# Kernel optimization log

Hardware: AMD Instinct MI355X
Metric: run time of the kernel (lower is better)

Reference implementation:

```python
import jax, jax.numpy as jnp
import numpy as np

H = 12
DH = 64
R = 8
LN_EPS = 1e-12


def setup_inputs() -> dict:
    key = jax.random.key(0)
    ks = jax.random.split(key, 6)
    B, T, D = 32, 512, 768
    s = 0.02  # realistic init scale so softmax/LN stay well-conditioned
    return {
        "hidden_states": jax.random.normal(ks[0], (B, T, D), jnp.float32),
        "Wq": jax.random.normal(ks[1], (D, D), jnp.float32) * s,
        "bq": jnp.zeros((D,), jnp.float32),
        "Wk": jax.random.normal(ks[2], (D, D), jnp.float32) * s,
        "bk": jnp.zeros((D,), jnp.float32),
        "Wv": jax.random.normal(ks[3], (D, D), jnp.float32) * s,
        "bv": jnp.zeros((D,), jnp.float32),
        "Wo": jax.random.normal(ks[4], (D, D), jnp.float32) * s,
        "bo": jnp.zeros((D,), jnp.float32),
        "ln_g": jnp.ones((D,), jnp.float32),
        "ln_b": jnp.zeros((D,), jnp.float32),
    }


def _bipartite_indices(metric, r):
    # metric: (B, T, dh); cosine-sim bipartite matching between even (a) and odd (b) tokens
    m = metric / (jnp.linalg.norm(metric, axis=-1, keepdims=True) + 1e-6)
    a, b = m[:, ::2], m[:, 1::2]
    scores = jnp.einsum('bad,bcd->bac', a, b)  # (B, Ta, Tb)
    node_max = scores.max(axis=-1)
    node_idx = scores.argmax(axis=-1)
    node_max = node_max.at[:, 0].set(-jnp.inf)  # protect CLS (a[0])
    r = min(r, a.shape[1] - 1)
    sorted_idx = jnp.argsort(-node_max, axis=-1)  # descending
    src_idx = sorted_idx[:, :r]
    unm_idx = sorted_idx[:, r:]
    dst_idx = jnp.take_along_axis(node_idx, src_idx, axis=-1)
    return src_idx, unm_idx, dst_idx


def _merge(x, src_idx, unm_idx, dst_idx):
    # x: (B, T, C) -> (B, T - r, C); scatter-mean matched even tokens into odd tokens
    src, dst = x[:, ::2], x[:, 1::2]
    matched = jnp.take_along_axis(src, src_idx[:, :, None], axis=1)  # (B, r, C)

    def scat(d, di, mm):
        sums = jnp.zeros_like(d).at[di].add(mm)
        cnt = jnp.zeros((d.shape[0],), d.dtype).at[di].add(jnp.ones(di.shape, d.dtype))
        # torch scatter_reduce 'mean' with include_self=True: (self + sum) / (1 + count)
        return (d + sums) / (1.0 + cnt[:, None])

    dst = jax.vmap(scat)(dst, dst_idx, matched)
    unm = jnp.take_along_axis(src, unm_idx[:, :, None], axis=1)
    return jnp.concatenate([unm, dst], axis=1)


def reference(hidden_states, Wq, bq, Wk, bk, Wv, bv, Wo, bo, ln_g, ln_b):
    B, T, D = hidden_states.shape

    def split_heads(x):
        return x.reshape(B, T, H, DH).transpose(0, 2, 1, 3)  # (B, H, T, dh)

    residual = hidden_states
    q = split_heads(hidden_states @ Wq + bq)
    k = split_heads(hidden_states @ Wk + bk)
    v = split_heads(hidden_states @ Wv + bv)

    # ToMe: match on head-averaged keys (computed under no_grad in torch)
    metric = jax.lax.stop_gradient(k.mean(axis=1))  # (B, T, dh)
    src_idx, unm_idx, dst_idx = _bipartite_indices(metric, R)

    def merge_heads(x):
        Bx, Hx, Tx, dx = x.shape
        y = x.transpose(0, 2, 1, 3).reshape(Bx, Tx, Hx * dx)
        y = _merge(y, src_idx, unm_idx, dst_idx)
        return y.reshape(Bx, y.shape[1], Hx, dx).transpose(0, 2, 1, 3)

    q = merge_heads(q)
    k = merge_heads(k)
    v = merge_heads(v)
    residual = _merge(residual, src_idx, unm_idx, dst_idx)

    scores = jnp.einsum('bhqd,bhkd->bhqk', q, k) / jnp.sqrt(jnp.float32(DH))
    probs = jax.nn.softmax(scores, axis=-1)  # dropout is identity in eval
    ctx = jnp.einsum('bhqk,bhkd->bhqd', probs, v)
    T2 = ctx.shape[2]
    ctx = ctx.transpose(0, 2, 1, 3).reshape(B, T2, D)
    out = ctx @ Wo + bo

    x = out + residual
    mu = x.mean(axis=-1, keepdims=True)
    var = x.var(axis=-1, keepdims=True)
    return (x - mu) / jnp.sqrt(var + LN_EPS) * ln_g + ln_b
```

## Files before the change

kernel.cpp:

```cpp
#include <hip/hip_runtime.h>
#include <math.h>

#define BNUM 32
#define TT   512
#define DD   768
#define HH   12
#define DHH  64
#define RR   8
#define TSRC 256
#define UNM  248
#define TM   504
#define MROW 16128

typedef unsigned short u16;
typedef unsigned int   u32;
typedef __attribute__((ext_vector_type(8))) short bfrag;
typedef __attribute__((ext_vector_type(4))) float ffrag;
typedef __attribute__((ext_vector_type(2))) unsigned int u32x2;

__device__ __forceinline__ u16 f2bf(float f) {
  u32 u = __float_as_uint(f);
  u = (u + 0x7fffu + ((u >> 16) & 1u)) >> 16;
  return (u16)u;
}
__device__ __forceinline__ u32 pack2bf(float a, float b) {
  u32 ua = __float_as_uint(a), ub = __float_as_uint(b);
  ua += 0x7fffu + ((ua >> 16) & 1u);
  ub += 0x7fffu + ((ub >> 16) & 1u);
  return (ua >> 16) | (ub & 0xffff0000u);
}
__device__ __forceinline__ float bf2f(u16 v) {
  return __uint_as_float(((u32)v) << 16);
}

__device__ __forceinline__ void gl2lds16(const u16* g, u16* l) {
  __builtin_amdgcn_global_load_lds(
      (const __attribute__((address_space(1))) void*)(g),
      (__attribute__((address_space(3))) void*)(l), 16, 0, 0);
}

__global__ __launch_bounds__(256) void wkr_kernel(
    const float* __restrict__ Wk, const float* __restrict__ bk,
    float* __restrict__ Wkr, float* __restrict__ bkr) {
  int idx = blockIdx.x * 256 + threadIdx.x;
  int d = idx >> 6, j = idx & 63;
  float s = 0.f;
  #pragma unroll
  for (int h = 0; h < HH; ++h) s += Wk[(size_t)d * DD + h * DHH + j];
  Wkr[idx] = s * (1.f / 12.f);
  if (idx < 64) {
    float sb = 0.f;
    #pragma unroll
    for (int h = 0; h < HH; ++h) sb += bk[h * DHH + idx];
    bkr[idx] = sb * (1.f / 12.f);
  }
}

__global__ __launch_bounds__(256) void gemm_f32_kernel(
    const float* __restrict__ A, const float* __restrict__ W,
    const float* __restrict__ bias, float* __restrict__ C,
    int M, int N, int K) {
  __shared__ float As[32][68];
  __shared__ float Ws[32][68];
  const int t  = threadIdx.x;
  const int m0 = blockIdx.x * 64;
  const int tx = t & 15, ty = t >> 4;
  const int a_kk = t & 31;
  const int a_m  = t >> 5;
  const int w_n  = t & 63;
  const int w_k0 = t >> 6;

  float a_pre[8], w_pre[8];
  #pragma unroll
  for (int l = 0; l < 8; ++l)
    a_pre[l] = A[(size_t)(m0 + a_m + 8 * l) * K + a_kk];
  #pragma unroll
  for (int l = 0; l < 8; ++l)
    w_pre[l] = W[(size_t)(w_k0 * 8 + l) * N + w_n];

  float acc[4][4];
  #pragma unroll
  for (int i = 0; i < 4; ++i)
    #pragma unroll
    for (int j = 0; j < 4; ++j) acc[i][j] = 0.f;

  for (int k0 = 0; k0 < K; k0 += 32) {
    __syncthreads();
    #pragma unroll
    for (int l = 0; l < 8; ++l) As[a_kk][a_m + 8 * l] = a_pre[l];
    #pragma unroll
    for (int l = 0; l < 8; ++l) Ws[w_k0 * 8 + l][w_n] = w_pre[l];
    __syncthreads();
    if (k0 + 32 < K) {
      #pragma unroll
      for (int l = 0; l < 8; ++l)
        a_pre[l] = A[(size_t)(m0 + a_m + 8 * l) * K + k0 + 32 + a_kk];
      #pragma unroll
      for (int l = 0; l < 8; ++l)
        w_pre[l] = W[(size_t)(k0 + 32 + w_k0 * 8 + l) * N + w_n];
    }
    #pragma unroll
    for (int kk = 0; kk < 32; ++kk) {
      float4 a4 = *(const float4*)&As[kk][ty * 4];
      float4 w4 = *(const float4*)&Ws[kk][tx * 4];
      acc[0][0] += a4.x * w4.x; acc[0][1] += a4.x * w4.y;
      acc[0][2] += a4.x * w4.z; acc[0][3] += a4.x * w4.w;
      acc[1][0] += a4.y * w4.x; acc[1][1] += a4.y * w4.y;
      acc[1][2] += a4.y * w4.z; acc[1][3] += a4.y * w4.w;
      acc[2][0] += a4.z * w4.x; acc[2][1] += a4.z * w4.y;
      acc[2][2] += a4.z * w4.z; acc[2][3] += a4.z * w4.w;
      acc[3][0] += a4.w * w4.x; acc[3][1] += a4.w * w4.y;
      acc[3][2] += a4.w * w4.z; acc[3][3] += a4.w * w4.w;
    }
  }
  const float4 b4 = *(const float4*)&bias[tx * 4];
  #pragma unroll
  for (int i = 0; i < 4; ++i) {
    float4 v;
    v.x = acc[i][0] + b4.x; v.y = acc[i][1] + b4.y;
    v.z = acc[i][2] + b4.z; v.w = acc[i][3] + b4.w;
    *(float4*)&C[(size_t)(m0 + ty * 4 + i) * N + tx * 4] = v;
  }
}

__global__ __launch_bounds__(256) void wconv_kernel(
    const float* __restrict__ W0, const float* __restrict__ W1,
    const float* __restrict__ W2, const float* __restrict__ W3,
    u16* __restrict__ T0, u16* __restrict__ T1,
    u16* __restrict__ T2, u16* __restrict__ T3) {
  __shared__ float tile[64][65];
  int wi = blockIdx.z;
  const float* W = (wi == 0) ? W0 : (wi == 1) ? W1 : (wi == 2) ? W2 : W3;
  u16* T = (wi == 0) ? T0 : (wi == 1) ? T1 : (wi == 2) ? T2 : T3;
  int k0 = blockIdx.x * 64, n0 = blockIdx.y * 64;
  int t = threadIdx.x;
  int r = t >> 2, c4 = (t & 3) * 16;
  #pragma unroll
  for (int j = 0; j < 16; j += 4) {
    float4 v = *(const float4*)&W[(size_t)(k0 + r) * DD + n0 + c4 + j];
    tile[r][c4 + j] = v.x; tile[r][c4 + j + 1] = v.y;
    tile[r][c4 + j + 2] = v.z; tile[r][c4 + j + 3] = v.w;
  }
  __syncthreads();
  #pragma unroll
  for (int j = 0; j < 16; j += 2) {
    u32 p = (u32)f2bf(tile[c4 + j][r]) | ((u32)f2bf(tile[c4 + j + 1][r]) << 16);
    *(u32*)&T[(size_t)(n0 + r) * DD + k0 + c4 + j] = p;
  }
}

template <bool OUT_BF16, bool ADD_RES, bool ROW_BIAS, bool QK, bool ASHARE>
__global__ __launch_bounds__(256, 4) void mfma_gemm_kernel(
    const u16* __restrict__ A, const u16* __restrict__ BT,
    const float* __restrict__ bias, const float* __restrict__ bias2,
    const float* __restrict__ Res,
    float* __restrict__ Cf, u16* __restrict__ Cb, u16* __restrict__ Cb2,
    int M, int N, int K) {
  __shared__ u16 Als[2][128 * 32];
  __shared__ u16 Bls[2][128 * 32];
  const int t  = threadIdx.x;

  const int gx = gridDim.x, gy = gridDim.y;
  const int nwg = gx * gy;
  int id = blockIdx.x + blockIdx.y * gx;
  {
    const int qq = nwg >> 3, rr = nwg & 7;
    const int xcd = id & 7, pos = id >> 3;
    id = (xcd < rr) ? (xcd * (qq + 1) + pos)
                    : (rr * (qq + 1) + (xcd - rr) * qq + pos);
  }
  int bm, bn;
  if (ASHARE) { bm = id / gy; bn = id % gy; }
  else        { bm = id % gx; bn = id / gx; }
  const int m0 = bm * 128;
  const int n0 = bn * 128;

  const int lane = t & 63;
  const int w  = t >> 6;
  const int wm = w & 1, wn = w >> 1;
  const int q  = lane >> 4;
  const int lr = lane & 15;

  const int srow = lane >> 2;
  const int schk = (lane & 3) ^ ((lane >> 3) & 3);
  const u16* gA = A  + (size_t)(m0 + w * 32 + srow) * K + schk * 8;
  const u16* gB = BT + (size_t)(n0 + w * 32 + srow) * K + schk * 8;

  const int ceff = q ^ ((lr >> 1) & 3);

  const float* biasp = bias;
  u16* Cbp = Cb;
  int n0c = n0;
  if (QK && n0 >= DD) { biasp = bias2; Cbp = Cb2; n0c = n0 - DD; }

  ffrag acc[4][4];
  #pragma unroll
  for (int i = 0; i < 4; ++i)
    #pragma unroll
    for (int j = 0; j < 4; ++j) {
      acc[i][j].x = 0.f; acc[i][j].y = 0.f; acc[i][j].z = 0.f; acc[i][j].w = 0.f;
    }

  auto STAGE = [&](int buf, int k0) {
    #pragma unroll
    for (int i = 0; i < 2; ++i) {
      gl2lds16(gA + (size_t)(i * 16) * K + k0, &Als[buf][(w * 32 + i * 16) * 32]);
      gl2lds16(gB + (size_t)(i * 16) * K + k0, &Bls[buf][(w * 32 + i * 16) * 32]);
    }
  };

  STAGE(0, 0);
  __syncthreads();

  const int NK = K >> 5;
  for (int kt = 0; kt < NK; ++kt) {
    const int cur = kt & 1;
    if (kt + 1 < NK) STAGE(cur ^ 1, (kt + 1) << 5);

    bfrag af[4], bfv[4];
    #pragma unroll
    for (int mi = 0; mi < 4; ++mi)
      af[mi] = *(const bfrag*)&Als[cur][((wm * 4 + mi) * 64 + lr * 4 + ceff) * 8];
    #pragma unroll
    for (int ni = 0; ni < 4; ++ni)
      bfv[ni] = *(const bfrag*)&Bls[cur][((wn * 4 + ni) * 64 + lr * 4 + ceff) * 8];
    #pragma unroll
    for (int mi = 0; mi < 4; ++mi)
      #pragma unroll
      for (int ni = 0; ni < 4; ++ni)
        acc[mi][ni] = __builtin_amdgcn_mfma_f32_16x16x32_bf16(
            af[mi], bfv[ni], acc[mi][ni], 0, 0, 0);

    __syncthreads();
  }

  float bcol[4];
  if (!ROW_BIAS) {
    #pragma unroll
    for (int ni = 0; ni < 4; ++ni)
      bcol[ni] = biasp[n0c + wn * 64 + ni * 16 + lr];
  }

  #pragma unroll
  for (int mi = 0; mi < 4; ++mi) {
    #pragma unroll
    for (int ni = 0; ni < 4; ++ni) {
      int gcol = n0c + wn * 64 + ni * 16 + lr;
      #pragma unroll
      for (int r = 0; r < 4; ++r) {
        int grow = m0 + wm * 64 + mi * 16 + q * 4 + r;
        size_t off = (size_t)grow * N + gcol;
        float v = acc[mi][ni][r];
        v += ROW_BIAS ? bias[grow] : bcol[ni];
        if (ADD_RES) v += Res[off];
        if (OUT_BF16) Cbp[off] = f2bf(v);
        else          Cf[off] = v;
      }
    }
  }
}

__global__ __launch_bounds__(256) void tome_scores_kernel(
    const float* __restrict__ metric, float* __restrict__ node_max,
    int* __restrict__ node_idx) {
  __shared__ float Bs[128][68];
  const int blk = blockIdx.x;
  const int b = blk >> 3, g = blk & 7;
  const int t = threadIdx.x;
  const int r = t >> 3, cc = t & 7;
  const int arow = g * 32 + r;
  const float* Mb = metric + (size_t)b * TT * 64;

  float areg[64];
  float na = 0.f;
  #pragma unroll
  for (int d4 = 0; d4 < 16; ++d4) {
    float4 v = *(const float4*)&Mb[(size_t)(2 * arow) * 64 + d4 * 4];
    areg[4 * d4 + 0] = v.x; areg[4 * d4 + 1] = v.y;
    areg[4 * d4 + 2] = v.z; areg[4 * d4 + 3] = v.w;
    na += v.x * v.x; na += v.y * v.y; na += v.z * v.z; na += v.w * v.w;
  }
  float ia = 1.f / (sqrtf(na) + 1e-6f);
  #pragma unroll
  for (int d = 0; d < 64; ++d) areg[d] *= ia;

  float best = -INFINITY; int besti = 0;
  for (int p = 0; p < 2; ++p) {
    __syncthreads();
    if (t < 128) {
      int c = p * 128 + t;
      const float* src = &Mb[(size_t)(2 * c + 1) * 64];
      float nb = 0.f;
      #pragma unroll
      for (int d4 = 0; d4 < 16; ++d4) {
        float4 v = *(const float4*)&src[d4 * 4];
        *(float4*)&Bs[t][d4 * 4] = v;
        nb += v.x * v.x; nb += v.y * v.y; nb += v.z * v.z; nb += v.w * v.w;
      }
      float ib = 1.f / (sqrtf(nb) + 1e-6f);
      #pragma unroll
      for (int d4 = 0; d4 < 16; ++d4) {
        float4 v = *(float4*)&Bs[t][d4 * 4];
        v.x *= ib; v.y *= ib; v.z *= ib; v.w *= ib;
        *(float4*)&Bs[t][d4 * 4] = v;
      }
    }
    __syncthreads();
    for (int j = 0; j < 16; ++j) {
      int cl = cc + 8 * j;
      float s = 0.f;
      #pragma unroll
      for (int d4 = 0; d4 < 16; ++d4) {
        float4 bv = *(const float4*)&Bs[cl][d4 * 4];
        s += areg[4 * d4 + 0] * bv.x; s += areg[4 * d4 + 1] * bv.y;
        s += areg[4 * d4 + 2] * bv.z; s += areg[4 * d4 + 3] * bv.w;
      }
      int c = p * 128 + cl;
      if (s > best) { best = s; besti = c; }
    }
  }
  #pragma unroll
  for (int off = 1; off < 8; off <<= 1) {
    float bm = __shfl_xor(best, off);
    int   bi = __shfl_xor(besti, off);
    if (bm > best || (bm == best && bi < besti)) { best = bm; besti = bi; }
  }
  if (cc == 0) {
    node_max[b * TSRC + arow] = best;
    node_idx[b * TSRC + arow] = besti;
  }
}

__global__ __launch_bounds__(256) void tome_rank_kernel(
    const float* __restrict__ node_max, const int* __restrict__ node_idx,
    int* __restrict__ order_g, int* __restrict__ dst_g) {
  __shared__ float km[TSRC];
  __shared__ int ord[TSRC];
  int b = blockIdx.x, i = threadIdx.x;
  float best = (i == 0) ? -INFINITY : node_max[b * TSRC + i];
  km[i] = best;
  __syncthreads();
  float ki = km[i];
  int r = 0;
  for (int j = 0; j < TSRC; ++j) {
    float kj = km[j];
    if (kj > ki || (kj == ki && j < i)) ++r;
  }
  ord[r] = i;
  __syncthreads();
  order_g[b * TSRC + i] = ord[i];
  if (i < RR) dst_g[b * RR + i] = node_idx[b * TSRC + ord[i]];
}

__global__ __launch_bounds__(256) void merge_kernel(
    const float* __restrict__ X, const int* __restrict__ order,
    const int* __restrict__ dsti, float* __restrict__ Xm,
    u16* __restrict__ Xmb) {
  int row = blockIdx.x;
  int b = row / TM, t2 = row % TM;
  int c = threadIdx.x;
  const float* Xb = X + (size_t)b * TT * DD;
  float out[3];
  if (t2 < UNM) {
    int tok = 2 * order[b * TSRC + RR + t2];
    #pragma unroll
    for (int l = 0; l < 3; ++l) out[l] = Xb[(size_t)tok * DD + c + 256 * l];
  } else {
    int j = t2 - UNM;
    float cnt = 1.f;
    #pragma unroll
    for (int l = 0; l < 3; ++l) out[l] = Xb[(size_t)(2 * j + 1) * DD + c + 256 * l];
    for (int m = 0; m < RR; ++m) {
      if (dsti[b * RR + m] == j) {
        int tok = 2 * order[b * TSRC + m];
        #pragma unroll
        for (int l = 0; l < 3; ++l) out[l] += Xb[(size_t)tok * DD + c + 256 * l];
        cnt += 1.f;
      }
    }
    float inv = 1.f / cnt;
    #pragma unroll
    for (int l = 0; l < 3; ++l) out[l] *= inv;
  }
  #pragma unroll
  for (int l = 0; l < 3; ++l) {
    Xm[(size_t)row * DD + c + 256 * l]  = out[l];
    Xmb[(size_t)row * DD + c + 256 * l] = f2bf(out[l]);
  }
}

#define NQT 8
__global__ __launch_bounds__(256, 4) void attn_kernel(
    const u16* __restrict__ Q, const u16* __restrict__ K,
    const u16* __restrict__ VT, u16* __restrict__ ctx) {
  __shared__ u16 Kls[2][64][64];
  __shared__ u16 Vls[2][64][64];

  int blk = blockIdx.x;
  int bh = blk % (BNUM * HH);
  int qt = blk / (BNUM * HH);
  int h = bh % HH, b = bh / HH;
  const int t = threadIdx.x;
  const int lane = t & 63, w = t >> 6;
  const int lr = lane & 15, quad = lane >> 4;
  const int q0 = qt * 64;
  const size_t base = (size_t)b * TM * DD + (size_t)h * DHH;

  bfrag qf[2];
  {
    const u16* qp = Q + base + (size_t)(q0 + 16 * w + lr) * DD + quad * 8;
    qf[0] = *(const bfrag*)(qp);
    qf[1] = *(const bfrag*)(qp + 32);
  }

  const int srow = lane >> 3;
  const int schk = (lane & 7) ^ srow;
  const u16* Kg = K + base + (size_t)schk * 8;
  const u16* Vg0 = VT + (size_t)(h * DHH + w * 16 + srow) * MROW + (size_t)b * TM;
  const u16* Vg1 = Vg0 + (size_t)8 * MROW;

  const int cA = (quad)     ^ (lr & 7);
  const int cB = (quad + 4) ^ (lr & 7);
  const int vq = quad >> 1, vh = (quad & 1) * 4, lx = lr & 7;
  const int hx = (lr >> 3) << 2;

  float m_i = -INFINITY, l_i = 0.f;
  ffrag o[4];
  #pragma unroll
  for (int ni = 0; ni < 4; ++ni) {
    o[ni].x = 0.f; o[ni].y = 0.f; o[ni].z = 0.f; o[ni].w = 0.f;
  }

  auto STAGE = [&](int cur, int kt) {
    const int k0s = kt * 64;
    int t0 = k0s + w * 16 + srow;
    int t1 = t0 + 8;
    t0 = (t0 < TM) ? t0 : (TM - 1);
    t1 = (t1 < TM) ? t1 : (TM - 1);
    gl2lds16(Kg + (size_t)t0 * DD, &Kls[cur][w * 16][0]);
    gl2lds16(Kg + (size_t)t1 * DD, &Kls[cur][w * 16 + 8][0]);
    int tb = k0s + schk * 8;
    tb = (tb <= TM - 8) ? tb : (TM - 8);
    gl2lds16(Vg0 + tb, &Vls[cur][w * 16][0]);
    int tb2 = k0s + (schk ^ 4) * 8;
    tb2 = (tb2 <= TM - 8) ? tb2 : (TM - 8);
    gl2lds16(Vg1 + tb2, &Vls[cur][w * 16 + 8][0]);
  };

  STAGE(0, 0);
  __syncthreads();

  const float L2E = 1.4426950408889634f;
  const float C1  = 0.125f * 1.4426950408889634f;

  #pragma unroll
  for (int kt = 0; kt < NQT; ++kt) {
    const int cur = kt & 1;

    if (kt + 1 < NQT) STAGE(cur ^ 1, kt + 1);

    ffrag s4[4];
    __builtin_amdgcn_s_setprio(1);
    #pragma unroll
    for (int mi = 0; mi < 4; ++mi) {
      bfrag ka0 = *(const bfrag*)&Kls[cur][mi * 16 + lr][cA * 8];
      bfrag ka1 = *(const bfrag*)&Kls[cur][mi * 16 + lr][cB * 8];
      ffrag z; z.x = 0.f; z.y = 0.f; z.z = 0.f; z.w = 0.f;
      z = __builtin_amdgcn_mfma_f32_16x16x32_bf16(ka0, qf[0], z, 0, 0, 0);
      s4[mi] = __builtin_amdgcn_mfma_f32_16x16x32_bf16(ka1, qf[1], z, 0, 0, 0);
    }
    __builtin_amdgcn_s_setprio(0);

    if (kt == NQT - 1) {
      #pragma unroll
      for (int mi = 0; mi < 4; ++mi)
        #pragma unroll
        for (int r = 0; r < 4; ++r) {
          int rel = mi * 16 + quad * 4 + r;
          if (mi == 3)
            s4[mi][r] = (448 + rel < TM) ? s4[mi][r] : -INFINITY;
        }
    }

    float mx01 = fmaxf(fmaxf(s4[0][0], s4[0][1]), fmaxf(s4[0][2], s4[0][3]));
    float mx23 = fmaxf(fmaxf(s4[1][0], s4[1][1]), fmaxf(s4[1][2], s4[1][3]));
    float mx45 = fmaxf(fmaxf(s4[2][0], s4[2][1]), fmaxf(s4[2][2], s4[2][3]));
    float mx67 = fmaxf(fmaxf(s4[3][0], s4[3][1]), fmaxf(s4[3][2], s4[3][3]));
    float rmax = fmaxf(fmaxf(mx01, mx23), fmaxf(mx45, mx67));
    rmax = fmaxf(rmax, __shfl_xor(rmax, 16));
    rmax = fmaxf(rmax, __shfl_xor(rmax, 32));
    float pmax = rmax * 0.125f;

    if (!__all(pmax <= m_i + 8.f)) {
      float nm = fmaxf(m_i, pmax);
      float alpha = __builtin_amdgcn_exp2f((m_i - nm) * L2E);
      float al[4];
      #pragma unroll
      for (int r = 0; r < 4; ++r) al[r] = __shfl(alpha, quad * 4 + r);
      #pragma unroll
      for (int ni = 0; ni < 4; ++ni)
        #pragma unroll
        for (int r = 0; r < 4; ++r) o[ni][r] *= al[r];
      l_i *= alpha;
      m_i = nm;
    }
    float nml2 = m_i * L2E;

    float p[16];
    float pa0 = 0.f, pa1 = 0.f, pa2 = 0.f, pa3 = 0.f;
    #pragma unroll
    for (int mi = 0; mi < 4; ++mi)
      #pragma unroll
      for (int r = 0; r < 4; ++r) {
        float e = __builtin_amdgcn_exp2f(__builtin_fmaf(s4[mi][r], C1, -nml2));
        p[mi * 4 + r] = e;
        if (r == 0) pa0 += e; else if (r == 1) pa1 += e;
        else if (r == 2) pa2 += e; else pa3 += e;
      }
    float psum = (pa0 + pa1) + (pa2 + pa3);
    psum += __shfl_xor(psum, 16);
    psum += __shfl_xor(psum, 32);
    l_i += psum;

    u32 pk[8];
    #pragma unroll
    for (int mi = 0; mi < 4; ++mi) {
      pk[2 * mi]     = pack2bf(p[mi * 4 + 0], p[mi * 4 + 1]);
      pk[2 * mi + 1] = pack2bf(p[mi * 4 + 2], p[mi * 4 + 3]);
    }

    __builtin_amdgcn_s_setprio(1);
    #pragma unroll
    for (int mh = 0; mh < 2; ++mh) {
      union { u32 u[4]; bfrag f; } pa;
      pa.u[0] = pk[4 * mh + 0]; pa.u[1] = pk[4 * mh + 1];
      pa.u[2] = pk[4 * mh + 2]; pa.u[3] = pk[4 * mh + 3];
      const int c0 = ((4 * mh + vq) ^ lx ^ hx) * 8 + vh;
      const int c1 = ((4 * mh + 2 + vq) ^ lx ^ hx) * 8 + vh;
      #pragma unroll
      for (int ni = 0; ni < 4; ++ni) {
        const u16* vp = &Vls[cur][ni * 16 + lr][0];
        u32x2 v0 = *(const u32x2*)(vp + c0);
        u32x2 v1 = *(const u32x2*)(vp + c1);
        union { u32 u[4]; bfrag f; } vb;
        vb.u[0] = v0.x; vb.u[1] = v0.y; vb.u[2] = v1.x; vb.u[3] = v1.y;
        o[ni] = __builtin_amdgcn_mfma_f32_16x16x32_bf16(pa.f, vb.f, o[ni], 0, 0, 0);
      }
    }
    __builtin_amdgcn_s_setprio(0);

    __syncthreads();
  }

  float invl[4];
  #pragma unroll
  for (int r = 0; r < 4; ++r) {
    float lv = __shfl(l_i, quad * 4 + r);
    invl[r] = 1.f / lv;
  }
  #pragma unroll
  for (int r = 0; r < 4; ++r) {
    int row = q0 + 16 * w + quad * 4 + r;
    if (row < TM) {
      size_t g = base + (size_t)row * DD + lr;
      #pragma unroll
      for (int ni = 0; ni < 4; ++ni)
        ctx[g + ni * 16] = f2bf(o[ni][r] * invl[r]);
    }
  }
}

__global__ __launch_bounds__(256) void ln_kernel(
    float* __restrict__ Y, const float* __restrict__ g,
    const float* __restrict__ beta) {
  __shared__ float red[4];
  int row = blockIdx.x, t = threadIdx.x;
  size_t baseo = (size_t)row * DD;
  float x[3];
  #pragma unroll
  for (int l = 0; l < 3; ++l) x[l] = Y[baseo + t + 256 * l];
  float s = x[0] + x[1] + x[2];
  #pragma unroll
  for (int off = 32; off > 0; off >>= 1) s += __shfl_down(s, off, 64);
  if ((t & 63) == 0) red[t >> 6] = s;
  __syncthreads();
  float mu = (red[0] + red[1] + red[2] + red[3]) * (1.f / 768.f);
  __syncthreads();
  float d0 = x[0] - mu, d1 = x[1] - mu, d2 = x[2] - mu;
  float sq = d0 * d0 + d1 * d1 + d2 * d2;
  #pragma unroll
  for (int off = 32; off > 0; off >>= 1) sq += __shfl_down(sq, off, 64);
  if ((t & 63) == 0) red[t >> 6] = sq;
  __syncthreads();
  float var = (red[0] + red[1] + red[2] + red[3]) * (1.f / 768.f);
  float inv = rsqrtf(var + 1e-12f);
  #pragma unroll
  for (int l = 0; l < 3; ++l) {
    int c = t + 256 * l;
    Y[baseo + c] = (x[l] - mu) * inv * g[c] + beta[c];
  }
}

extern "C" void kernel_launch(void* const* d_in, const int* in_sizes, int n_in,
                              void* d_out, int out_size, void* d_ws, size_t ws_size,
                              hipStream_t stream) {
  const float* X    = (const float*)d_in[0];
  const float* Wq   = (const float*)d_in[1];
  const float* bq   = (const float*)d_in[2];
  const float* Wk   = (const float*)d_in[3];
  const float* bk   = (const float*)d_in[4];
  const float* Wv   = (const float*)d_in[5];
  const float* bv   = (const float*)d_in[6];
  const float* Wo   = (const float*)d_in[7];
  const float* bo   = (const float*)d_in[8];
  const float* ln_g = (const float*)d_in[9];
  const float* ln_b = (const float*)d_in[10];
  float* out = (float*)d_out;

  const size_t metric_n = (size_t)16384 * 64;
  const size_t wkr_n    = (size_t)768 * 64 + 64;
  const size_t idx_n    = (size_t)BNUM * TSRC + BNUM * RR;
  const size_t nm_n     = (size_t)2 * BNUM * TSRC;
  const size_t buf_n    = (size_t)MROW * DD;
  const size_t w_n      = (size_t)DD * DD;
  const size_t f32_elems = metric_n + wkr_n + idx_n + nm_n + buf_n;
  const size_t u16_elems = 4 * buf_n + 4 * w_n;
  const size_t needed = f32_elems * 4 + u16_elems * 2;
  if (ws_size < needed) return;

  float* ws = (float*)d_ws;
  float* metric   = ws;
  float* Wkr      = metric + metric_n;
  float* bkr      = Wkr + (size_t)768 * 64;
  int*   order_g  = (int*)(bkr + 64);
  int*   dst_g    = order_g + BNUM * TSRC;
  float* node_max = (float*)(dst_g + BNUM * RR);
  int*   node_idx = (int*)(node_max + BNUM * TSRC);
  float* Xm       = (float*)(node_idx + BNUM * TSRC);
  u16*   Xmb      = (u16*)(Xm + buf_n);
  u16*   Qmb      = Xmb + buf_n;
  u16*   Kmb      = Qmb + buf_n;
  u16*   VTb      = Kmb + buf_n;
  u16*   WqT      = VTb + buf_n;
  u16*   WkT      = WqT + w_n;
  u16*   WvT      = WkT + w_n;
  u16*   WoT      = WvT + w_n;
  u16*   ctxb     = Qmb;

  wkr_kernel<<<(768 * 64) / 256, 256, 0, stream>>>(Wk, bk, Wkr, bkr);
  wconv_kernel<<<dim3(12, 12, 4), 256, 0, stream>>>(
      Wq, Wk, Wv, Wo, WqT, WkT, WvT, WoT);
  gemm_f32_kernel<<<dim3(16384 / 64, 1), 256, 0, stream>>>(
      X, Wkr, bkr, metric, 16384, 64, 768);
  tome_scores_kernel<<<BNUM * 8, 256, 0, stream>>>(metric, node_max, node_idx);
  tome_rank_kernel<<<BNUM, 256, 0, stream>>>(node_max, node_idx, order_g, dst_g);
  merge_kernel<<<MROW, 256, 0, stream>>>(X, order_g, dst_g, Xm, Xmb);
  mfma_gemm_kernel<true, false, false, true, true>
      <<<dim3(MROW / 128, 2 * DD / 128), 256, 0, stream>>>(
      Xmb, WqT, bq, bk, nullptr, nullptr, Qmb, Kmb, MROW, DD, DD);
  mfma_gemm_kernel<true, false, true, false, false>
      <<<dim3(DD / 128, MROW / 128), 256, 0, stream>>>(
      WvT, Xmb, bv, nullptr, nullptr, nullptr, VTb, nullptr, DD, MROW, DD);
  attn_kernel<<<BNUM * HH * NQT, 256, 0, stream>>>(Qmb, Kmb, VTb, ctxb);
  mfma_gemm_kernel<false, true, false, false, true>
      <<<dim3(MROW / 128, DD / 128), 256, 0, stream>>>(
      ctxb, WoT, bo, nullptr, Xm, out, nullptr, nullptr, MROW, DD, DD);
  ln_kernel<<<MROW, 256, 0, stream>>>(out, ln_g, ln_b);
}
```

Measured before the change: 372.4 us.

## Use 256x128 GEMM tiles with 512 threads, remap attention blocks, use hardware bf16 pack

```diff
diff --git a/kernel.cpp b/kernel.cpp
--- a/kernel.cpp
+++ b/kernel.cpp
@@ -23,14 +23,16 @@
   u = (u + 0x7fffu + ((u >> 16) & 1u)) >> 16;
   return (u16)u;
 }
-__device__ __forceinline__ u32 pack2bf(float a, float b) {
-  u32 ua = __float_as_uint(a), ub = __float_as_uint(b);
-  ua += 0x7fffu + ((ua >> 16) & 1u);
-  ub += 0x7fffu + ((ub >> 16) & 1u);
-  return (ua >> 16) | (ub & 0xffff0000u);
+__device__ __forceinline__ u32 cvtpk2bf(float a, float b) {
+  u32 r;
+  asm("v_cvt_pk_bf16_f32 %0, %1, %2" : "=v"(r) : "v"(a), "v"(b));
+  return r;
 }
 __device__ __forceinline__ float bf2f(u16 v) {
   return __uint_as_float(((u32)v) << 16);
+}
+__device__ __forceinline__ float max3f(float a, float b, float c) {
+  return fmaxf(fmaxf(a, b), c);
 }
 
 __device__ __forceinline__ void gl2lds16(const u16* g, u16* l) {
@@ -150,13 +152,13 @@
 }
 
 template <bool OUT_BF16, bool ADD_RES, bool ROW_BIAS, bool QK, bool ASHARE>
-__global__ __launch_bounds__(256, 4) void mfma_gemm_kernel(
+__global__ __launch_bounds__(512, 4) void mfma_gemm_kernel(
     const u16* __restrict__ A, const u16* __restrict__ BT,
     const float* __restrict__ bias, const float* __restrict__ bias2,
     const float* __restrict__ Res,
     float* __restrict__ Cf, u16* __restrict__ Cb, u16* __restrict__ Cb2,
     int M, int N, int K) {
-  __shared__ u16 Als[2][128 * 32];
+  __shared__ u16 Als[2][256 * 32];
   __shared__ u16 Bls[2][128 * 32];
   const int t  = threadIdx.x;
 
@@ -172,19 +174,19 @@
   int bm, bn;
   if (ASHARE) { bm = id / gy; bn = id % gy; }
   else        { bm = id % gx; bn = id / gx; }
-  const int m0 = bm * 128;
+  const int m0 = bm * 256;
   const int n0 = bn * 128;
 
   const int lane = t & 63;
   const int w  = t >> 6;
-  const int wm = w & 1, wn = w >> 1;
+  const int wm = w & 3, wn = w >> 2;
   const int q  = lane >> 4;
   const int lr = lane & 15;
 
   const int srow = lane >> 2;
   const int schk = (lane & 3) ^ ((lane >> 3) & 3);
   const u16* gA = A  + (size_t)(m0 + w * 32 + srow) * K + schk * 8;
-  const u16* gB = BT + (size_t)(n0 + w * 32 + srow) * K + schk * 8;
+  const u16* gB = BT + (size_t)(n0 + w * 16 + srow) * K + schk * 8;
 
   const int ceff = q ^ ((lr >> 1) & 3);
 
@@ -203,10 +205,9 @@
 
   auto STAGE = [&](int buf, int k0) {
     #pragma unroll
-    for (int i = 0; i < 2; ++i) {
+    for (int i = 0; i < 2; ++i)
       gl2lds16(gA + (size_t)(i * 16) * K + k0, &Als[buf][(w * 32 + i * 16) * 32]);
-      gl2lds16(gB + (size_t)(i * 16) * K + k0, &Bls[buf][(w * 32 + i * 16) * 32]);
-    }
+    gl2lds16(gB + k0, &Bls[buf][(w * 16) * 32]);
   };
 
   STAGE(0, 0);
@@ -397,8 +398,9 @@
   __shared__ u16 Vls[2][64][64];
 
   int blk = blockIdx.x;
-  int bh = blk % (BNUM * HH);
-  int qt = blk / (BNUM * HH);
+  int pos = blk >> 3, xcd = blk & 7;
+  int qt = pos & 7;
+  int bh = xcd * 48 + (pos >> 3);
   int h = bh % HH, b = bh / HH;
   const int t = threadIdx.x;
   const int lane = t & 63, w = t >> 6;
@@ -482,11 +484,12 @@
         }
     }
 
-    float mx01 = fmaxf(fmaxf(s4[0][0], s4[0][1]), fmaxf(s4[0][2], s4[0][3]));
-    float mx23 = fmaxf(fmaxf(s4[1][0], s4[1][1]), fmaxf(s4[1][2], s4[1][3]));
-    float mx45 = fmaxf(fmaxf(s4[2][0], s4[2][1]), fmaxf(s4[2][2], s4[2][3]));
-    float mx67 = fmaxf(fmaxf(s4[3][0], s4[3][1]), fmaxf(s4[3][2], s4[3][3]));
-    float rmax = fmaxf(fmaxf(mx01, mx23), fmaxf(mx45, mx67));
+    float ma = max3f(s4[0][0], s4[0][1], s4[0][2]);
+    float mb = max3f(s4[0][3], s4[1][0], s4[1][1]);
+    float mc = max3f(s4[1][2], s4[1][3], s4[2][0]);
+    float md = max3f(s4[2][1], s4[2][2], s4[2][3]);
+    float me = max3f(s4[3][0], s4[3][1], s4[3][2]);
+    float rmax = max3f(fmaxf(ma, mb), fmaxf(mc, md), fmaxf(me, s4[3][3]));
     rmax = fmaxf(rmax, __shfl_xor(rmax, 16));
     rmax = fmaxf(rmax, __shfl_xor(rmax, 32));
     float pmax = rmax * 0.125f;
@@ -525,8 +528,8 @@
     u32 pk[8];
     #pragma unroll
     for (int mi = 0; mi < 4; ++mi) {
-      pk[2 * mi]     = pack2bf(p[mi * 4 + 0], p[mi * 4 + 1]);
-      pk[2 * mi + 1] = pack2bf(p[mi * 4 + 2], p[mi * 4 + 3]);
+      pk[2 * mi]     = cvtpk2bf(p[mi * 4 + 0], p[mi * 4 + 1]);
+      pk[2 * mi + 1] = cvtpk2bf(p[mi * 4 + 2], p[mi * 4 + 3]);
     }
 
     __builtin_amdgcn_s_setprio(1);
@@ -656,14 +659,14 @@
   tome_rank_kernel<<<BNUM, 256, 0, stream>>>(node_max, node_idx, order_g, dst_g);
   merge_kernel<<<MROW, 256, 0, stream>>>(X, order_g, dst_g, Xm, Xmb);
   mfma_gemm_kernel<true, false, false, true, true>
-      <<<dim3(MROW / 128, 2 * DD / 128), 256, 0, stream>>>(
+      <<<dim3(MROW / 256, 2 * DD / 128), 512, 0, stream>>>(
       Xmb, WqT, bq, bk, nullptr, nullptr, Qmb, Kmb, MROW, DD, DD);
   mfma_gemm_kernel<true, false, true, false, false>
-      <<<dim3(DD / 128, MROW / 128), 256, 0, stream>>>(
+      <<<dim3(DD / 256, MROW / 128), 512, 0, stream>>>(
       WvT, Xmb, bv, nullptr, nullptr, nullptr, VTb, nullptr, DD, MROW, DD);
   attn_kernel<<<BNUM * HH * NQT, 256, 0, stream>>>(Qmb, Kmb, VTb, ctxb);
   mfma_gemm_kernel<false, true, false, false, true>
-      <<<dim3(MROW / 128, DD / 128), 256, 0, stream>>>(
+      <<<dim3(MROW / 256, DD / 128), 512, 0, stream>>>(
       ctxb, WoT, bo, nullptr, Xm, out, nullptr, nullptr, MROW, DD, DD);
   ln_kernel<<<MROW, 256, 0, stream>>>(out, ln_g, ln_b);
 }
```

After: 367.6 us. Within noise of the previous version (-1.3%).
